# Kernel optimization log

Hardware: AMD Instinct MI355X
Metric: run time of the kernel (lower is better)

Reference implementation:

```python
import jax, jax.numpy as jnp
import numpy as np


def setup_inputs() -> dict:
    key = jax.random.key(0)
    k1, k2 = jax.random.split(key)
    B, S, H = 8, 2048, 1024
    lstm_output = jax.random.normal(k1, (B, S, H), dtype=jnp.float32)
    # xavier-uniform-like init for the bilinear weight
    limit = float(np.sqrt(6.0 / (H + H)))
    attention_weights = jax.random.uniform(k2, (H, H), dtype=jnp.float32, minval=-limit, maxval=limit)
    return {"lstm_output": lstm_output, "attention_weights": attention_weights}


def reference(lstm_output, attention_weights):
    # scores[b,i,j] = (x[b,i] @ W) . x[b,j]
    xw = jnp.einsum('bsh,hk->bsk', lstm_output, attention_weights)      # [B,S,H]
    scores = jnp.einsum('bsk,btk->bst', xw, lstm_output)                # [B,S,S]
    attn = jax.nn.softmax(scores, axis=-1)                              # [B,S,S]
    context = jnp.einsum('bst,bth->bsh', attn, lstm_output)             # [B,S,H]
    return (context, attn)
```

## Files before the change

kernel.cpp:

```cpp
#include <hip/hip_runtime.h>
#include <hip/hip_bf16.h>


#define BB 8
#define SS 2048
#define HH 1024

typedef __attribute__((ext_vector_type(8))) short bf16x8;
typedef __attribute__((ext_vector_type(4))) float f32x4;

__device__ __forceinline__ void async_load16(const void* gsrc, void* ldst) {
    typedef const unsigned int __attribute__((address_space(1)))* gp_t;
    typedef unsigned int __attribute__((address_space(3)))* lp_t;
    __builtin_amdgcn_global_load_lds((gp_t)gsrc, (lp_t)ldst, 16, 0, 0);
}

__device__ __forceinline__ unsigned short f2b(float f) {
    __hip_bfloat16 h = __float2bfloat16(f);
    return *(unsigned short*)&h;
}
__device__ __forceinline__ float b2f(unsigned short u) {
    __hip_bfloat16 h = *(__hip_bfloat16*)&u;
    return __bfloat162float(h);
}

__global__ __launch_bounds__(256) void split_x(const float* __restrict__ X,
                                               unsigned short* __restrict__ Xh,
                                               unsigned short* __restrict__ Xl) {
    const size_t i = ((size_t)blockIdx.x * 256 + threadIdx.x) * 8;
    float4 a = *(const float4*)(X + i);
    float4 b = *(const float4*)(X + i + 4);
    ushort4 h0, h1, l0, l1;
    float v, hf;
    v = a.x; h0.x = f2b(v); hf = b2f(h0.x); l0.x = f2b(v - hf);
    v = a.y; h0.y = f2b(v); hf = b2f(h0.y); l0.y = f2b(v - hf);
    v = a.z; h0.z = f2b(v); hf = b2f(h0.z); l0.z = f2b(v - hf);
    v = a.w; h0.w = f2b(v); hf = b2f(h0.w); l0.w = f2b(v - hf);
    v = b.x; h1.x = f2b(v); hf = b2f(h1.x); l1.x = f2b(v - hf);
    v = b.y; h1.y = f2b(v); hf = b2f(h1.y); l1.y = f2b(v - hf);
    v = b.z; h1.z = f2b(v); hf = b2f(h1.z); l1.z = f2b(v - hf);
    v = b.w; h1.w = f2b(v); hf = b2f(h1.w); l1.w = f2b(v - hf);
    *(ushort4*)(Xh + i) = h0; *(ushort4*)(Xh + i + 4) = h1;
    *(ushort4*)(Xl + i) = l0; *(ushort4*)(Xl + i + 4) = l1;
}

__global__ __launch_bounds__(256) void split_wT(const float* __restrict__ W,
                                                unsigned short* __restrict__ Th,
                                                unsigned short* __restrict__ Tl) {
    const int k0 = blockIdx.y * 64, n0 = blockIdx.x * 64;
    __shared__ float tile[64][65];
#pragma unroll
    for (int q = 0; q < 16; q++) {
        int idx = q * 256 + threadIdx.x;
        int r = idx >> 6, c = idx & 63;
        tile[r][c] = W[(size_t)(k0 + r) * HH + n0 + c];
    }
    __syncthreads();
#pragma unroll
    for (int q = 0; q < 16; q++) {
        int idx = q * 256 + threadIdx.x;
        int r = idx >> 6, c = idx & 63;
        float v = tile[c][r];
        unsigned short h = f2b(v);
        Th[(size_t)(n0 + r) * HH + k0 + c] = h;
        Tl[(size_t)(n0 + r) * HH + k0 + c] = f2b(v - b2f(h));
    }
}

__global__ __launch_bounds__(256) void gemm_xw3(const unsigned short* __restrict__ Ah,
                                                const unsigned short* __restrict__ Al,
                                                const unsigned short* __restrict__ Bh,
                                                const unsigned short* __restrict__ Bl,
                                                unsigned short* __restrict__ Ch,
                                                unsigned short* __restrict__ Cl) {
    const int b = blockIdx.z;
    const int i0 = blockIdx.y * 128, n0 = blockIdx.x * 128;
    const unsigned short* A_h = Ah + (size_t)b * SS * HH;
    const unsigned short* A_l = Al + (size_t)b * SS * HH;

    __shared__ __align__(16) unsigned short AsH[128 * 32];
    __shared__ __align__(16) unsigned short AsL[128 * 32];
    __shared__ __align__(16) unsigned short BsH[128 * 32];
    __shared__ __align__(16) unsigned short BsL[128 * 32];

    const int tid = threadIdx.x;
    const int wave = tid >> 6, lane = tid & 63;
    const int m16 = lane & 15, quad = lane >> 4;
    const int wy = wave >> 1, wx = wave & 1;
    const int rowA = tid >> 2;
    const int kq = (tid & 3) ^ ((rowA >> 1) & 3);

    f32x4 acc[4][4] = {};

    for (int k0 = 0; k0 < HH; k0 += 32) {
        const size_t ga0 = (size_t)(i0 + rowA) * HH + k0 + kq * 8;
        const size_t ga1 = (size_t)(i0 + 64 + rowA) * HH + k0 + kq * 8;
        const size_t gb0 = (size_t)(n0 + rowA) * HH + k0 + kq * 8;
        const size_t gb1 = (size_t)(n0 + 64 + rowA) * HH + k0 + kq * 8;
        async_load16(A_h + ga0, (char*)AsH + wave * 1024);
        async_load16(A_h + ga1, (char*)AsH + 4096 + wave * 1024);
        async_load16(A_l + ga0, (char*)AsL + wave * 1024);
        async_load16(A_l + ga1, (char*)AsL + 4096 + wave * 1024);
        async_load16(Bh + gb0, (char*)BsH + wave * 1024);
        async_load16(Bh + gb1, (char*)BsH + 4096 + wave * 1024);
        async_load16(Bl + gb0, (char*)BsL + wave * 1024);
        async_load16(Bl + gb1, (char*)BsL + 4096 + wave * 1024);
        __syncthreads();

        const int cs = quad ^ ((m16 >> 1) & 3);
        const int offA = (wy * 64 + m16) * 32 + cs * 8;
        const int offB = (wx * 64 + m16) * 32 + cs * 8;
        bf16x8 ah[4], al[4], bh[4], bl[4];
#pragma unroll
        for (int r = 0; r < 4; r++) {
            ah[r] = *(const bf16x8*)(AsH + offA + r * 16 * 32);
            al[r] = *(const bf16x8*)(AsL + offA + r * 16 * 32);
        }
#pragma unroll
        for (int c = 0; c < 4; c++) {
            bh[c] = *(const bf16x8*)(BsH + offB + c * 16 * 32);
            bl[c] = *(const bf16x8*)(BsL + offB + c * 16 * 32);
        }
#pragma unroll
        for (int r = 0; r < 4; r++)
#pragma unroll
            for (int c = 0; c < 4; c++) {
                acc[r][c] = __builtin_amdgcn_mfma_f32_16x16x32_bf16(ah[r], bh[c], acc[r][c], 0, 0, 0);
                acc[r][c] = __builtin_amdgcn_mfma_f32_16x16x32_bf16(ah[r], bl[c], acc[r][c], 0, 0, 0);
                acc[r][c] = __builtin_amdgcn_mfma_f32_16x16x32_bf16(al[r], bh[c], acc[r][c], 0, 0, 0);
            }
        __syncthreads();
    }

    unsigned short* ChB = Ch + (size_t)b * SS * HH;
    unsigned short* ClB = Cl + (size_t)b * SS * HH;
#pragma unroll
    for (int r = 0; r < 4; r++) {
        const int row = i0 + wy * 64 + r * 16 + quad * 4;
#pragma unroll
        for (int c = 0; c < 4; c++) {
            const int col = n0 + wx * 64 + c * 16 + m16;
#pragma unroll
            for (int reg = 0; reg < 4; reg++) {
                float v = acc[r][c][reg];
                unsigned short h = f2b(v);
                ChB[(size_t)(row + reg) * HH + col] = h;
                ClB[(size_t)(row + reg) * HH + col] = f2b(v - b2f(h));
            }
        }
    }
}

__global__ __launch_bounds__(512, 2) void gemm_sc3_8p(const unsigned short* __restrict__ Ah,
                                                      const unsigned short* __restrict__ Al,
                                                      const unsigned short* __restrict__ Bh,
                                                      const unsigned short* __restrict__ Bl,
                                                      float* __restrict__ SC) {
    const int b = blockIdx.z;
    const int i0 = blockIdx.y * 256, j0 = blockIdx.x * 256;
    const unsigned short* A_h = Ah + (size_t)b * SS * HH;
    const unsigned short* A_l = Al + (size_t)b * SS * HH;
    const unsigned short* B_h = Bh + (size_t)b * SS * HH;
    const unsigned short* B_l = Bl + (size_t)b * SS * HH;

    __shared__ __align__(16) unsigned short lds[65536];

    const int tid = threadIdx.x;
    const int wave = tid >> 6, lane = tid & 63;
    const int m16 = lane & 15, quad = lane >> 4;
    const int wy = wave >> 2, wx = wave & 3;
    const int rP = tid >> 2;
    const int kq = (tid & 3) ^ ((rP >> 1) & 3);
    const int cs = quad ^ ((m16 >> 1) & 3);
    const int wt16 = wave * 1024;
    const int rowA_off = (rP & 63) + ((rP >> 6) << 7);
    const int rowB_off = ((rP >> 5) << 6) + (rP & 31);

    const size_t aOff = (size_t)(i0 + rowA_off) * HH + kq * 8;
    const size_t bOff = (size_t)(j0 + rowB_off) * HH + kq * 8;

    f32x4 acc[2][4][2][2] = {};
    bf16x8 a_h[4], a_l[4], b_h[2][2], b_l[2][2];

#define STG_A(mh, kt, buf) do { \
        const size_t o_ = aOff + (size_t)(mh) * 64 * HH + (size_t)(kt) * 32; \
        async_load16(A_h + o_, (char*)lds + ((buf) * 32768 + (mh) * 4096) * 2 + wt16); \
        async_load16(A_l + o_, (char*)lds + ((buf) * 32768 + 8192 + (mh) * 4096) * 2 + wt16); \
    } while (0)
#define STG_B(nh, kt, buf) do { \
        const size_t o_ = bOff + (size_t)(nh) * 32 * HH + (size_t)(kt) * 32; \
        async_load16(B_h + o_, (char*)lds + ((buf) * 32768 + 16384 + (nh) * 4096) * 2 + wt16); \
        async_load16(B_l + o_, (char*)lds + ((buf) * 32768 + 24576 + (nh) * 4096) * 2 + wt16); \
    } while (0)
#define RD_A(mh, buf) do { \
        const int s0_ = (buf) * 32768 + ((mh) * 128 + wy * 64 + m16) * 32 + cs * 8; \
        _Pragma("unroll") for (int mi = 0; mi < 4; ++mi) { \
            a_h[mi] = *(const bf16x8*)&lds[s0_ + mi * 512]; \
            a_l[mi] = *(const bf16x8*)&lds[8192 + s0_ + mi * 512]; \
        } } while (0)
#define RD_B(nh, buf) do { \
        const int s0_ = (buf) * 32768 + ((nh) * 128 + wx * 32 + m16) * 32 + cs * 8; \
        _Pragma("unroll") for (int nj = 0; nj < 2; ++nj) { \
            b_h[nh][nj] = *(const bf16x8*)&lds[16384 + s0_ + nj * 512]; \
            b_l[nh][nj] = *(const bf16x8*)&lds[24576 + s0_ + nj * 512]; \
        } } while (0)
#define MFMA_PH(mh, nh) \
        __builtin_amdgcn_s_setprio(1); \
        _Pragma("unroll") for (int mi = 0; mi < 4; ++mi) \
        _Pragma("unroll") for (int nj = 0; nj < 2; ++nj) { \
            acc[mh][mi][nh][nj] = __builtin_amdgcn_mfma_f32_16x16x32_bf16(a_h[mi], b_h[nh][nj], acc[mh][mi][nh][nj], 0, 0, 0); \
            acc[mh][mi][nh][nj] = __builtin_amdgcn_mfma_f32_16x16x32_bf16(a_h[mi], b_l[nh][nj], acc[mh][mi][nh][nj], 0, 0, 0); \
            acc[mh][mi][nh][nj] = __builtin_amdgcn_mfma_f32_16x16x32_bf16(a_l[mi], b_h[nh][nj], acc[mh][mi][nh][nj], 0, 0, 0); \
        } \
        __builtin_amdgcn_s_setprio(0);

    STG_A(0, 0, 0); STG_A(1, 0, 0);
    STG_B(0, 0, 0); STG_B(1, 0, 0);
    STG_B(0, 1, 1); STG_B(1, 1, 1);
    asm volatile("s_waitcnt vmcnt(4)" ::: "memory");
    __builtin_amdgcn_s_barrier();
    RD_B(0, 0); RD_B(1, 0);

    for (int kt = 0; kt < 32; ++kt) {
        const int bufc = kt & 1, bufn = bufc ^ 1;
        const int ktA = kt < 31 ? kt + 1 : 31;
        const int ktB = kt < 30 ? kt + 2 : 31;
        RD_A(0, bufc);
        STG_A(0, ktA, bufn);
        __builtin_amdgcn_s_barrier();
        __builtin_amdgcn_sched_barrier(0);
        MFMA_PH(0, 0)
        __builtin_amdgcn_sched_barrier(0);
        __builtin_amdgcn_s_barrier();
        asm volatile("s_waitcnt vmcnt(6)" ::: "memory");
        STG_A(1, ktA, bufn);
        __builtin_amdgcn_s_barrier();
        __builtin_amdgcn_sched_barrier(0);
        MFMA_PH(0, 1)
        __builtin_amdgcn_sched_barrier(0);
        __builtin_amdgcn_s_barrier();
        asm volatile("s_waitcnt vmcnt(6)" ::: "memory");
        RD_A(1, bufc);
        STG_B(0, ktB, bufc);
        __builtin_amdgcn_s_barrier();
        __builtin_amdgcn_sched_barrier(0);
        MFMA_PH(1, 0)
        __builtin_amdgcn_sched_barrier(0);
        RD_B(0, bufn);
        __builtin_amdgcn_s_barrier();
        asm volatile("s_waitcnt vmcnt(4)" ::: "memory");
        STG_B(1, ktB, bufc);
        __builtin_amdgcn_s_barrier();
        __builtin_amdgcn_sched_barrier(0);
        MFMA_PH(1, 1)
        __builtin_amdgcn_sched_barrier(0);
        RD_B(1, bufn);
        __builtin_amdgcn_s_barrier();
    }

    float* Cb = SC + (size_t)b * SS * SS;
#pragma unroll
    for (int mh = 0; mh < 2; ++mh)
#pragma unroll
        for (int mi = 0; mi < 4; ++mi)
#pragma unroll
            for (int nh = 0; nh < 2; ++nh)
#pragma unroll
                for (int nj = 0; nj < 2; ++nj) {
                    const int row = i0 + wy * 128 + mh * 64 + mi * 16 + quad * 4;
                    const int col = j0 + wx * 64 + nh * 32 + nj * 16 + m16;
#pragma unroll
                    for (int reg = 0; reg < 4; ++reg)
                        Cb[(size_t)(row + reg) * SS + col] = acc[mh][mi][nh][nj][reg];
                }
#undef STG_A
#undef STG_B
#undef RD_A
#undef RD_B
#undef MFMA_PH
}

__global__ __launch_bounds__(256) void softmax_rows(float* __restrict__ P,
                                                    unsigned short* __restrict__ Pb) {
    const size_t row = blockIdx.x;
    float4* p4 = (float4*)(P + row * SS);
    const int tid = threadIdx.x;
    float4 v0 = p4[tid], v1 = p4[tid + 256];
    float m = fmaxf(fmaxf(fmaxf(v0.x, v0.y), fmaxf(v0.z, v0.w)),
                    fmaxf(fmaxf(v1.x, v1.y), fmaxf(v1.z, v1.w)));
#pragma unroll
    for (int off = 32; off; off >>= 1) m = fmaxf(m, __shfl_xor(m, off));
    __shared__ float red[4];
    const int wid = tid >> 6, lane = tid & 63;
    if (lane == 0) red[wid] = m;
    __syncthreads();
    m = fmaxf(fmaxf(red[0], red[1]), fmaxf(red[2], red[3]));
    v0.x = __expf(v0.x - m); v0.y = __expf(v0.y - m);
    v0.z = __expf(v0.z - m); v0.w = __expf(v0.w - m);
    v1.x = __expf(v1.x - m); v1.y = __expf(v1.y - m);
    v1.z = __expf(v1.z - m); v1.w = __expf(v1.w - m);
    float s = v0.x + v0.y + v0.z + v0.w + v1.x + v1.y + v1.z + v1.w;
#pragma unroll
    for (int off = 32; off; off >>= 1) s += __shfl_xor(s, off);
    __syncthreads();
    if (lane == 0) red[wid] = s;
    __syncthreads();
    s = red[0] + red[1] + red[2] + red[3];
    const float inv = 1.0f / s;
    v0.x *= inv; v0.y *= inv; v0.z *= inv; v0.w *= inv;
    v1.x *= inv; v1.y *= inv; v1.z *= inv; v1.w *= inv;
    p4[tid] = v0;
    p4[tid + 256] = v1;
    ushort4* b4 = (ushort4*)(Pb + row * SS);
    ushort4 u0 = { f2b(v0.x), f2b(v0.y), f2b(v0.z), f2b(v0.w) };
    ushort4 u1 = { f2b(v1.x), f2b(v1.y), f2b(v1.z), f2b(v1.w) };
    b4[tid] = u0;
    b4[tid + 256] = u1;
}

__global__ __launch_bounds__(256) void transpose_cvt(const float* __restrict__ X,
                                                     unsigned short* __restrict__ XT) {
    const int b = blockIdx.z;
    const int t0 = blockIdx.y * 64;
    const int h0 = blockIdx.x * 64;
    __shared__ float tile[64][65];
    const float* Xb = X + (size_t)b * SS * HH;
    unsigned short* Tb = XT + (size_t)b * HH * SS;
#pragma unroll
    for (int q = 0; q < 16; q++) {
        int idx = q * 256 + threadIdx.x;
        int r = idx >> 6, c = idx & 63;
        tile[r][c] = Xb[(size_t)(t0 + r) * HH + h0 + c];
    }
    __syncthreads();
#pragma unroll
    for (int q = 0; q < 16; q++) {
        int idx = q * 256 + threadIdx.x;
        int r = idx >> 6, c = idx & 63;
        Tb[(size_t)(h0 + r) * SS + t0 + c] = f2b(tile[c][r]);
    }
}

__global__ __launch_bounds__(256) void gemm_ctx_mfma(const unsigned short* __restrict__ Ab,
                                                     const unsigned short* __restrict__ Bt,
                                                     float* __restrict__ C) {
    const int b = blockIdx.z;
    const int i0 = blockIdx.y * 128;
    const int n0 = blockIdx.x * 128;
    const unsigned short* A = Ab + (size_t)b * SS * SS;
    const unsigned short* B = Bt + (size_t)b * HH * SS;

    __shared__ __align__(16) unsigned short As[128 * 32];
    __shared__ __align__(16) unsigned short Bs[128 * 32];

    const int tid = threadIdx.x;
    const int wave = tid >> 6, lane = tid & 63;
    const int m16 = lane & 15, quad = lane >> 4;
    const int wy = wave >> 1, wx = wave & 1;
    const int rowA = tid >> 2;
    const int kq = (tid & 3) ^ ((rowA >> 1) & 3);

    f32x4 acc[4][4] = {};

    for (int k0 = 0; k0 < SS; k0 += 32) {
        async_load16(A + (size_t)(i0 + rowA) * SS + k0 + kq * 8, (char*)As + wave * 1024);
        async_load16(A + (size_t)(i0 + 64 + rowA) * SS + k0 + kq * 8, (char*)As + 4096 + wave * 1024);
        async_load16(B + (size_t)(n0 + rowA) * SS + k0 + kq * 8, (char*)Bs + wave * 1024);
        async_load16(B + (size_t)(n0 + 64 + rowA) * SS + k0 + kq * 8, (char*)Bs + 4096 + wave * 1024);
        __syncthreads();

        const int cs = quad ^ ((m16 >> 1) & 3);
        const unsigned short* pA = As + (wy * 64 + m16) * 32 + cs * 8;
        const unsigned short* pB = Bs + (wx * 64 + m16) * 32 + cs * 8;
        bf16x8 af[4], bfr[4];
#pragma unroll
        for (int r = 0; r < 4; r++) af[r] = *(const bf16x8*)(pA + r * 16 * 32);
#pragma unroll
        for (int c = 0; c < 4; c++) bfr[c] = *(const bf16x8*)(pB + c * 16 * 32);
#pragma unroll
        for (int r = 0; r < 4; r++)
#pragma unroll
            for (int c = 0; c < 4; c++)
                acc[r][c] = __builtin_amdgcn_mfma_f32_16x16x32_bf16(af[r], bfr[c], acc[r][c], 0, 0, 0);
        __syncthreads();
    }

    float* Cb = C + (size_t)b * SS * HH;
#pragma unroll
    for (int r = 0; r < 4; r++) {
        const int row = i0 + wy * 64 + r * 16 + quad * 4;
#pragma unroll
        for (int c = 0; c < 4; c++) {
            const int col = n0 + wx * 64 + c * 16 + m16;
#pragma unroll
            for (int reg = 0; reg < 4; reg++)
                Cb[(size_t)(row + reg) * HH + col] = acc[r][c][reg];
        }
    }
}

extern "C" void kernel_launch(void* const* d_in, const int* in_sizes, int n_in,
                              void* d_out, int out_size, void* d_ws, size_t ws_size,
                              hipStream_t stream) {
    const float* X = (const float*)d_in[0];
    const float* W = (const float*)d_in[1];
    float* ctx  = (float*)d_out;
    float* attn = ctx + (size_t)BB * SS * HH;

    char* ws = (char*)d_ws;
    unsigned short* x_hi  = (unsigned short*)ws;
    unsigned short* x_lo  = (unsigned short*)(ws + ((size_t)32 << 20));
    unsigned short* wt_hi = (unsigned short*)(ws + ((size_t)64 << 20));
    unsigned short* wt_lo = (unsigned short*)(ws + ((size_t)66 << 20));
    unsigned short* xT     = x_hi;
    unsigned short* attn_b = x_lo;

    unsigned short* xw_hi = (unsigned short*)d_out;
    unsigned short* xw_lo = xw_hi + (size_t)BB * SS * HH;

    dim3 blk(256);
    split_x <<<dim3(BB * SS * HH / (8 * 256)), blk, 0, stream>>>(X, x_hi, x_lo);
    split_wT<<<dim3(HH / 64, HH / 64), blk, 0, stream>>>(W, wt_hi, wt_lo);
    gemm_xw3<<<dim3(HH / 128, SS / 128, BB), blk, 0, stream>>>(x_hi, x_lo, wt_hi, wt_lo, xw_hi, xw_lo);
    gemm_sc3_8p<<<dim3(SS / 256, SS / 256, BB), dim3(512), 0, stream>>>(xw_hi, xw_lo, x_hi, x_lo, attn);
    transpose_cvt<<<dim3(HH / 64, SS / 64, BB), blk, 0, stream>>>(X, xT);
    softmax_rows <<<dim3(BB * SS), blk, 0, stream>>>(attn, attn_b);
    gemm_ctx_mfma<<<dim3(HH / 128, SS / 128, BB), blk, 0, stream>>>(attn_b, xT, ctx);
}
```

Measured before the change: 679.8 us.

## Port XW and context GEMMs to the 256x256 eight-wave pipelined MFMA kernel

The XW projection and the context GEMM move from simple 128x128 single-buffered kernels onto the same 256x256, 512-thread, double-buffered, phase-interleaved pipeline already used for the score GEMM. That pipeline issues async global-to-LDS loads ahead of use, uses s_setprio around MFMA bursts, and gives each thread a larger output tile. The goal is to hide load latency, remove the per-k-step full barriers of the old kernels and raise data reuse per LDS byte. In exchange the kernels need more registers and LDS, and the grids get smaller (e.g. 4x8x8 blocks), which may leave fewer waves to fill the device.

Result: faster. 608.8 us (-10.5%).

```diff
diff --git a/kernel.cpp b/kernel.cpp
--- a/kernel.cpp
+++ b/kernel.cpp
@@ -67,101 +67,18 @@
     }
 }
 
-__global__ __launch_bounds__(256) void gemm_xw3(const unsigned short* __restrict__ Ah,
-                                                const unsigned short* __restrict__ Al,
-                                                const unsigned short* __restrict__ Bh,
-                                                const unsigned short* __restrict__ Bl,
-                                                unsigned short* __restrict__ Ch,
-                                                unsigned short* __restrict__ Cl) {
-    const int b = blockIdx.z;
-    const int i0 = blockIdx.y * 128, n0 = blockIdx.x * 128;
-    const unsigned short* A_h = Ah + (size_t)b * SS * HH;
-    const unsigned short* A_l = Al + (size_t)b * SS * HH;
-
-    __shared__ __align__(16) unsigned short AsH[128 * 32];
-    __shared__ __align__(16) unsigned short AsL[128 * 32];
-    __shared__ __align__(16) unsigned short BsH[128 * 32];
-    __shared__ __align__(16) unsigned short BsL[128 * 32];
-
-    const int tid = threadIdx.x;
-    const int wave = tid >> 6, lane = tid & 63;
-    const int m16 = lane & 15, quad = lane >> 4;
-    const int wy = wave >> 1, wx = wave & 1;
-    const int rowA = tid >> 2;
-    const int kq = (tid & 3) ^ ((rowA >> 1) & 3);
-
-    f32x4 acc[4][4] = {};
-
-    for (int k0 = 0; k0 < HH; k0 += 32) {
-        const size_t ga0 = (size_t)(i0 + rowA) * HH + k0 + kq * 8;
-        const size_t ga1 = (size_t)(i0 + 64 + rowA) * HH + k0 + kq * 8;
-        const size_t gb0 = (size_t)(n0 + rowA) * HH + k0 + kq * 8;
-        const size_t gb1 = (size_t)(n0 + 64 + rowA) * HH + k0 + kq * 8;
-        async_load16(A_h + ga0, (char*)AsH + wave * 1024);
-        async_load16(A_h + ga1, (char*)AsH + 4096 + wave * 1024);
-        async_load16(A_l + ga0, (char*)AsL + wave * 1024);
-        async_load16(A_l + ga1, (char*)AsL + 4096 + wave * 1024);
-        async_load16(Bh + gb0, (char*)BsH + wave * 1024);
-        async_load16(Bh + gb1, (char*)BsH + 4096 + wave * 1024);
-        async_load16(Bl + gb0, (char*)BsL + wave * 1024);
-        async_load16(Bl + gb1, (char*)BsL + 4096 + wave * 1024);
-        __syncthreads();
-
-        const int cs = quad ^ ((m16 >> 1) & 3);
-        const int offA = (wy * 64 + m16) * 32 + cs * 8;
-        const int offB = (wx * 64 + m16) * 32 + cs * 8;
-        bf16x8 ah[4], al[4], bh[4], bl[4];
-#pragma unroll
-        for (int r = 0; r < 4; r++) {
-            ah[r] = *(const bf16x8*)(AsH + offA + r * 16 * 32);
-            al[r] = *(const bf16x8*)(AsL + offA + r * 16 * 32);
-        }
-#pragma unroll
-        for (int c = 0; c < 4; c++) {
-            bh[c] = *(const bf16x8*)(BsH + offB + c * 16 * 32);
-            bl[c] = *(const bf16x8*)(BsL + offB + c * 16 * 32);
-        }
-#pragma unroll
-        for (int r = 0; r < 4; r++)
-#pragma unroll
-            for (int c = 0; c < 4; c++) {
-                acc[r][c] = __builtin_amdgcn_mfma_f32_16x16x32_bf16(ah[r], bh[c], acc[r][c], 0, 0, 0);
-                acc[r][c] = __builtin_amdgcn_mfma_f32_16x16x32_bf16(ah[r], bl[c], acc[r][c], 0, 0, 0);
-                acc[r][c] = __builtin_amdgcn_mfma_f32_16x16x32_bf16(al[r], bh[c], acc[r][c], 0, 0, 0);
-            }
-        __syncthreads();
-    }
-
-    unsigned short* ChB = Ch + (size_t)b * SS * HH;
-    unsigned short* ClB = Cl + (size_t)b * SS * HH;
-#pragma unroll
-    for (int r = 0; r < 4; r++) {
-        const int row = i0 + wy * 64 + r * 16 + quad * 4;
-#pragma unroll
-        for (int c = 0; c < 4; c++) {
-            const int col = n0 + wx * 64 + c * 16 + m16;
-#pragma unroll
-            for (int reg = 0; reg < 4; reg++) {
-                float v = acc[r][c][reg];
-                unsigned short h = f2b(v);
-                ChB[(size_t)(row + reg) * HH + col] = h;
-                ClB[(size_t)(row + reg) * HH + col] = f2b(v - b2f(h));
-            }
-        }
-    }
-}
-
-__global__ __launch_bounds__(512, 2) void gemm_sc3_8p(const unsigned short* __restrict__ Ah,
+__global__ __launch_bounds__(512, 2) void gemm_xw3_8p(const unsigned short* __restrict__ Ah,
                                                       const unsigned short* __restrict__ Al,
                                                       const unsigned short* __restrict__ Bh,
                                                       const unsigned short* __restrict__ Bl,
-                                                      float* __restrict__ SC) {
+                                                      unsigned short* __restrict__ Ch,
+                                                      unsigned short* __restrict__ Cl) {
     const int b = blockIdx.z;
     const int i0 = blockIdx.y * 256, j0 = blockIdx.x * 256;
     const unsigned short* A_h = Ah + (size_t)b * SS * HH;
     const unsigned short* A_l = Al + (size_t)b * SS * HH;
-    const unsigned short* B_h = Bh + (size_t)b * SS * HH;
-    const unsigned short* B_l = Bl + (size_t)b * SS * HH;
+    const unsigned short* B_h = Bh;
+    const unsigned short* B_l = Bl;
 
     __shared__ __align__(16) unsigned short lds[65536];
 
@@ -258,6 +175,140 @@
         __builtin_amdgcn_s_barrier();
     }
 
+    unsigned short* ChB = Ch + (size_t)b * SS * HH;
+    unsigned short* ClB = Cl + (size_t)b * SS * HH;
+#pragma unroll
+    for (int mh = 0; mh < 2; ++mh)
+#pragma unroll
+        for (int mi = 0; mi < 4; ++mi)
+#pragma unroll
+            for (int nh = 0; nh < 2; ++nh)
+#pragma unroll
+                for (int nj = 0; nj < 2; ++nj) {
+                    const int row = i0 + wy * 128 + mh * 64 + mi * 16 + quad * 4;
+                    const int col = j0 + wx * 64 + nh * 32 + nj * 16 + m16;
+#pragma unroll
+                    for (int reg = 0; reg < 4; ++reg) {
+                        float v = acc[mh][mi][nh][nj][reg];
+                        unsigned short h = f2b(v);
+                        ChB[(size_t)(row + reg) * HH + col] = h;
+                        ClB[(size_t)(row + reg) * HH + col] = f2b(v - b2f(h));
+                    }
+                }
+#undef STG_A
+#undef STG_B
+#undef RD_A
+#undef RD_B
+#undef MFMA_PH
+}
+
+__global__ __launch_bounds__(512, 2) void gemm_sc3_8p(const unsigned short* __restrict__ Ah,
+                                                      const unsigned short* __restrict__ Al,
+                                                      const unsigned short* __restrict__ Bh,
+                                                      const unsigned short* __restrict__ Bl,
+                                                      float* __restrict__ SC) {
+    const int b = blockIdx.z;
+    const int i0 = blockIdx.y * 256, j0 = blockIdx.x * 256;
+    const unsigned short* A_h = Ah + (size_t)b * SS * HH;
+    const unsigned short* A_l = Al + (size_t)b * SS * HH;
+    const unsigned short* B_h = Bh + (size_t)b * SS * HH;
+    const unsigned short* B_l = Bl + (size_t)b * SS * HH;
+
+    __shared__ __align__(16) unsigned short lds[65536];
+
+    const int tid = threadIdx.x;
+    const int wave = tid >> 6, lane = tid & 63;
+    const int m16 = lane & 15, quad = lane >> 4;
+    const int wy = wave >> 2, wx = wave & 3;
+    const int rP = tid >> 2;
+    const int kq = (tid & 3) ^ ((rP >> 1) & 3);
+    const int cs = quad ^ ((m16 >> 1) & 3);
+    const int wt16 = wave * 1024;
+    const int rowA_off = (rP & 63) + ((rP >> 6) << 7);
+    const int rowB_off = ((rP >> 5) << 6) + (rP & 31);
+
+    const size_t aOff = (size_t)(i0 + rowA_off) * HH + kq * 8;
+    const size_t bOff = (size_t)(j0 + rowB_off) * HH + kq * 8;
+
+    f32x4 acc[2][4][2][2] = {};
+    bf16x8 a_h[4], a_l[4], b_h[2][2], b_l[2][2];
+
+#define STG_A(mh, kt, buf) do { \
+        const size_t o_ = aOff + (size_t)(mh) * 64 * HH + (size_t)(kt) * 32; \
+        async_load16(A_h + o_, (char*)lds + ((buf) * 32768 + (mh) * 4096) * 2 + wt16); \
+        async_load16(A_l + o_, (char*)lds + ((buf) * 32768 + 8192 + (mh) * 4096) * 2 + wt16); \
+    } while (0)
+#define STG_B(nh, kt, buf) do { \
+        const size_t o_ = bOff + (size_t)(nh) * 32 * HH + (size_t)(kt) * 32; \
+        async_load16(B_h + o_, (char*)lds + ((buf) * 32768 + 16384 + (nh) * 4096) * 2 + wt16); \
+        async_load16(B_l + o_, (char*)lds + ((buf) * 32768 + 24576 + (nh) * 4096) * 2 + wt16); \
+    } while (0)
+#define RD_A(mh, buf) do { \
+        const int s0_ = (buf) * 32768 + ((mh) * 128 + wy * 64 + m16) * 32 + cs * 8; \
+        _Pragma("unroll") for (int mi = 0; mi < 4; ++mi) { \
+            a_h[mi] = *(const bf16x8*)&lds[s0_ + mi * 512]; \
+            a_l[mi] = *(const bf16x8*)&lds[8192 + s0_ + mi * 512]; \
+        } } while (0)
+#define RD_B(nh, buf) do { \
+        const int s0_ = (buf) * 32768 + ((nh) * 128 + wx * 32 + m16) * 32 + cs * 8; \
+        _Pragma("unroll") for (int nj = 0; nj < 2; ++nj) { \
+            b_h[nh][nj] = *(const bf16x8*)&lds[16384 + s0_ + nj * 512]; \
+            b_l[nh][nj] = *(const bf16x8*)&lds[24576 + s0_ + nj * 512]; \
+        } } while (0)
+#define MFMA_PH(mh, nh) \
+        __builtin_amdgcn_s_setprio(1); \
+        _Pragma("unroll") for (int mi = 0; mi < 4; ++mi) \
+        _Pragma("unroll") for (int nj = 0; nj < 2; ++nj) { \
+            acc[mh][mi][nh][nj] = __builtin_amdgcn_mfma_f32_16x16x32_bf16(a_h[mi], b_h[nh][nj], acc[mh][mi][nh][nj], 0, 0, 0); \
+            acc[mh][mi][nh][nj] = __builtin_amdgcn_mfma_f32_16x16x32_bf16(a_h[mi], b_l[nh][nj], acc[mh][mi][nh][nj], 0, 0, 0); \
+            acc[mh][mi][nh][nj] = __builtin_amdgcn_mfma_f32_16x16x32_bf16(a_l[mi], b_h[nh][nj], acc[mh][mi][nh][nj], 0, 0, 0); \
+        } \
+        __builtin_amdgcn_s_setprio(0);
+
+    STG_A(0, 0, 0); STG_A(1, 0, 0);
+    STG_B(0, 0, 0); STG_B(1, 0, 0);
+    STG_B(0, 1, 1); STG_B(1, 1, 1);
+    asm volatile("s_waitcnt vmcnt(4)" ::: "memory");
+    __builtin_amdgcn_s_barrier();
+    RD_B(0, 0); RD_B(1, 0);
+
+    for (int kt = 0; kt < 32; ++kt) {
+        const int bufc = kt & 1, bufn = bufc ^ 1;
+        const int ktA = kt < 31 ? kt + 1 : 31;
+        const int ktB = kt < 30 ? kt + 2 : 31;
+        RD_A(0, bufc);
+        STG_A(0, ktA, bufn);
+        __builtin_amdgcn_s_barrier();
+        __builtin_amdgcn_sched_barrier(0);
+        MFMA_PH(0, 0)
+        __builtin_amdgcn_sched_barrier(0);
+        __builtin_amdgcn_s_barrier();
+        asm volatile("s_waitcnt vmcnt(6)" ::: "memory");
+        STG_A(1, ktA, bufn);
+        __builtin_amdgcn_s_barrier();
+        __builtin_amdgcn_sched_barrier(0);
+        MFMA_PH(0, 1)
+        __builtin_amdgcn_sched_barrier(0);
+        __builtin_amdgcn_s_barrier();
+        asm volatile("s_waitcnt vmcnt(6)" ::: "memory");
+        RD_A(1, bufc);
+        STG_B(0, ktB, bufc);
+        __builtin_amdgcn_s_barrier();
+        __builtin_amdgcn_sched_barrier(0);
+        MFMA_PH(1, 0)
+        __builtin_amdgcn_sched_barrier(0);
+        RD_B(0, bufn);
+        __builtin_amdgcn_s_barrier();
+        asm volatile("s_waitcnt vmcnt(4)" ::: "memory");
+        STG_B(1, ktB, bufc);
+        __builtin_amdgcn_s_barrier();
+        __builtin_amdgcn_sched_barrier(0);
+        MFMA_PH(1, 1)
+        __builtin_amdgcn_sched_barrier(0);
+        RD_B(1, bufn);
+        __builtin_amdgcn_s_barrier();
+    }
+
     float* Cb = SC + (size_t)b * SS * SS;
 #pragma unroll
     for (int mh = 0; mh < 2; ++mh)
@@ -341,62 +392,127 @@
     }
 }
 
-__global__ __launch_bounds__(256) void gemm_ctx_mfma(const unsigned short* __restrict__ Ab,
-                                                     const unsigned short* __restrict__ Bt,
-                                                     float* __restrict__ C) {
+__global__ __launch_bounds__(512, 2) void gemm_ctx_8p(const unsigned short* __restrict__ Ab,
+                                                      const unsigned short* __restrict__ Bt,
+                                                      float* __restrict__ C) {
     const int b = blockIdx.z;
-    const int i0 = blockIdx.y * 128;
-    const int n0 = blockIdx.x * 128;
+    const int i0 = blockIdx.y * 256, n0 = blockIdx.x * 256;
     const unsigned short* A = Ab + (size_t)b * SS * SS;
     const unsigned short* B = Bt + (size_t)b * HH * SS;
 
-    __shared__ __align__(16) unsigned short As[128 * 32];
-    __shared__ __align__(16) unsigned short Bs[128 * 32];
+    __shared__ __align__(16) unsigned short lds[65536];
 
     const int tid = threadIdx.x;
     const int wave = tid >> 6, lane = tid & 63;
     const int m16 = lane & 15, quad = lane >> 4;
-    const int wy = wave >> 1, wx = wave & 1;
-    const int rowA = tid >> 2;
-    const int kq = (tid & 3) ^ ((rowA >> 1) & 3);
-
-    f32x4 acc[4][4] = {};
-
-    for (int k0 = 0; k0 < SS; k0 += 32) {
-        async_load16(A + (size_t)(i0 + rowA) * SS + k0 + kq * 8, (char*)As + wave * 1024);
-        async_load16(A + (size_t)(i0 + 64 + rowA) * SS + k0 + kq * 8, (char*)As + 4096 + wave * 1024);
-        async_load16(B + (size_t)(n0 + rowA) * SS + k0 + kq * 8, (char*)Bs + wave * 1024);
-        async_load16(B + (size_t)(n0 + 64 + rowA) * SS + k0 + kq * 8, (char*)Bs + 4096 + wave * 1024);
-        __syncthreads();
-
-        const int cs = quad ^ ((m16 >> 1) & 3);
-        const unsigned short* pA = As + (wy * 64 + m16) * 32 + cs * 8;
-        const unsigned short* pB = Bs + (wx * 64 + m16) * 32 + cs * 8;
-        bf16x8 af[4], bfr[4];
-#pragma unroll
-        for (int r = 0; r < 4; r++) af[r] = *(const bf16x8*)(pA + r * 16 * 32);
-#pragma unroll
-        for (int c = 0; c < 4; c++) bfr[c] = *(const bf16x8*)(pB + c * 16 * 32);
-#pragma unroll
-        for (int r = 0; r < 4; r++)
-#pragma unroll
-            for (int c = 0; c < 4; c++)
-                acc[r][c] = __builtin_amdgcn_mfma_f32_16x16x32_bf16(af[r], bfr[c], acc[r][c], 0, 0, 0);
-        __syncthreads();
+    const int m7 = m16 & 7;
+    const int wy = wave >> 2, wx = wave & 3;
+    const int rA8 = tid >> 3;
+    const int c8 = (tid & 7) ^ (rA8 & 7);
+    const int wt16 = wave * 1024;
+    const int sl0 = (quad ^ m7) * 8;
+    const int sl1 = ((quad + 4) ^ m7) * 8;
+
+    const size_t aSrc = (size_t)(i0 + rA8) * SS + c8 * 8;
+    const size_t bSrc = (size_t)(n0 + ((rA8 >> 5) << 6) + (rA8 & 31)) * SS + c8 * 8;
+
+    f32x4 acc[2][4][2][2] = {};
+    bf16x8 a[4][2], bb[2][2][2];
+
+#define CSTG_A(mh, h, kt, buf) \
+    async_load16(A + aSrc + (size_t)((mh) * 64 + (h) * 128) * SS + (size_t)(kt) * 64, \
+                 (char*)lds + (buf) * 65536 + (mh) * 16384 + (h) * 8192 + wt16)
+#define CSTG_B(nh, h, kt, buf) \
+    async_load16(B + bSrc + (size_t)((h) * 128 + (nh) * 32) * SS + (size_t)(kt) * 64, \
+                 (char*)lds + (buf) * 65536 + 32768 + (nh) * 16384 + (h) * 8192 + wt16)
+#define CRD_A(mh, buf) do { \
+        const int r0_ = (buf) * 32768 + ((mh) * 128 + wy * 64 + m16) * 64; \
+        _Pragma("unroll") for (int mi = 0; mi < 4; ++mi) { \
+            a[mi][0] = *(const bf16x8*)&lds[r0_ + mi * 1024 + sl0]; \
+            a[mi][1] = *(const bf16x8*)&lds[r0_ + mi * 1024 + sl1]; \
+        } } while (0)
+#define CRD_B(nh, buf) do { \
+        const int r0_ = (buf) * 32768 + 16384 + (nh) * 8192 + (wx * 32 + m16) * 64; \
+        _Pragma("unroll") for (int nj = 0; nj < 2; ++nj) { \
+            bb[nh][nj][0] = *(const bf16x8*)&lds[r0_ + nj * 1024 + sl0]; \
+            bb[nh][nj][1] = *(const bf16x8*)&lds[r0_ + nj * 1024 + sl1]; \
+        } } while (0)
+#define CMFMA(mh, nh) \
+        __builtin_amdgcn_s_setprio(1); \
+        _Pragma("unroll") for (int mi = 0; mi < 4; ++mi) \
+        _Pragma("unroll") for (int nj = 0; nj < 2; ++nj) { \
+            acc[mh][mi][nh][nj] = __builtin_amdgcn_mfma_f32_16x16x32_bf16(a[mi][0], bb[nh][nj][0], acc[mh][mi][nh][nj], 0, 0, 0); \
+            acc[mh][mi][nh][nj] = __builtin_amdgcn_mfma_f32_16x16x32_bf16(a[mi][1], bb[nh][nj][1], acc[mh][mi][nh][nj], 0, 0, 0); \
+        } \
+        __builtin_amdgcn_s_setprio(0);
+
+    CSTG_A(0, 0, 0, 0); CSTG_A(0, 1, 0, 0);
+    CSTG_A(1, 0, 0, 0); CSTG_A(1, 1, 0, 0);
+    CSTG_B(0, 0, 0, 0); CSTG_B(0, 1, 0, 0);
+    CSTG_B(1, 0, 0, 0); CSTG_B(1, 1, 0, 0);
+    CSTG_B(0, 0, 1, 1); CSTG_B(0, 1, 1, 1);
+    CSTG_B(1, 0, 1, 1); CSTG_B(1, 1, 1, 1);
+    asm volatile("s_waitcnt vmcnt(4)" ::: "memory");
+    __builtin_amdgcn_s_barrier();
+    CRD_B(0, 0); CRD_B(1, 0);
+
+    for (int kt = 0; kt < 32; ++kt) {
+        const int bufc = kt & 1, bufn = bufc ^ 1;
+        const int ktA = kt < 31 ? kt + 1 : 31;
+        const int ktB = kt < 30 ? kt + 2 : 31;
+        CRD_A(0, bufc);
+        CSTG_A(0, 0, ktA, bufn); CSTG_A(0, 1, ktA, bufn);
+        __builtin_amdgcn_s_barrier();
+        __builtin_amdgcn_sched_barrier(0);
+        CMFMA(0, 0)
+        __builtin_amdgcn_sched_barrier(0);
+        __builtin_amdgcn_s_barrier();
+        asm volatile("s_waitcnt vmcnt(6)" ::: "memory");
+        CSTG_A(1, 0, ktA, bufn); CSTG_A(1, 1, ktA, bufn);
+        __builtin_amdgcn_s_barrier();
+        __builtin_amdgcn_sched_barrier(0);
+        CMFMA(0, 1)
+        __builtin_amdgcn_sched_barrier(0);
+        __builtin_amdgcn_s_barrier();
+        asm volatile("s_waitcnt vmcnt(6)" ::: "memory");
+        CRD_A(1, bufc);
+        CSTG_B(0, 0, ktB, bufc); CSTG_B(0, 1, ktB, bufc);
+        __builtin_amdgcn_s_barrier();
+        __builtin_amdgcn_sched_barrier(0);
+        CMFMA(1, 0)
+        __builtin_amdgcn_sched_barrier(0);
+        CRD_B(0, bufn);
+        __builtin_amdgcn_s_barrier();
+        asm volatile("s_waitcnt vmcnt(4)" ::: "memory");
+        CSTG_B(1, 0, ktB, bufc); CSTG_B(1, 1, ktB, bufc);
+        __builtin_amdgcn_s_barrier();
+        __builtin_amdgcn_sched_barrier(0);
+        CMFMA(1, 1)
+        __builtin_amdgcn_sched_barrier(0);
+        CRD_B(1, bufn);
+        __builtin_amdgcn_s_barrier();
     }
 
     float* Cb = C + (size_t)b * SS * HH;
 #pragma unroll
-    for (int r = 0; r < 4; r++) {
-        const int row = i0 + wy * 64 + r * 16 + quad * 4;
-#pragma unroll
-        for (int c = 0; c < 4; c++) {
-            const int col = n0 + wx * 64 + c * 16 + m16;
-#pragma unroll
-            for (int reg = 0; reg < 4; reg++)
-                Cb[(size_t)(row + reg) * HH + col] = acc[r][c][reg];
-        }
-    }
+    for (int mh = 0; mh < 2; ++mh)
+#pragma unroll
+        for (int mi = 0; mi < 4; ++mi)
+#pragma unroll
+            for (int nh = 0; nh < 2; ++nh)
+#pragma unroll
+                for (int nj = 0; nj < 2; ++nj) {
+                    const int row = i0 + wy * 128 + mh * 64 + mi * 16 + quad * 4;
+                    const int col = n0 + wx * 64 + nh * 32 + nj * 16 + m16;
+#pragma unroll
+                    for (int reg = 0; reg < 4; ++reg)
+                        Cb[(size_t)(row + reg) * HH + col] = acc[mh][mi][nh][nj][reg];
+                }
+#undef CSTG_A
+#undef CSTG_B
+#undef CRD_A
+#undef CRD_B
+#undef CMFMA
 }
 
 extern "C" void kernel_launch(void* const* d_in, const int* in_sizes, int n_in,
@@ -421,9 +537,9 @@
     dim3 blk(256);
     split_x <<<dim3(BB * SS * HH / (8 * 256)), blk, 0, stream>>>(X, x_hi, x_lo);
     split_wT<<<dim3(HH / 64, HH / 64), blk, 0, stream>>>(W, wt_hi, wt_lo);
-    gemm_xw3<<<dim3(HH / 128, SS / 128, BB), blk, 0, stream>>>(x_hi, x_lo, wt_hi, wt_lo, xw_hi, xw_lo);
+    gemm_xw3_8p<<<dim3(HH / 256, SS / 256, BB), dim3(512), 0, stream>>>(x_hi, x_lo, wt_hi, wt_lo, xw_hi, xw_lo);
     gemm_sc3_8p<<<dim3(SS / 256, SS / 256, BB), dim3(512), 0, stream>>>(xw_hi, xw_lo, x_hi, x_lo, attn);
     transpose_cvt<<<dim3(HH / 64, SS / 64, BB), blk, 0, stream>>>(X, xT);
     softmax_rows <<<dim3(BB * SS), blk, 0, stream>>>(attn, attn_b);
-    gemm_ctx_mfma<<<dim3(HH / 128, SS / 128, BB), blk, 0, stream>>>(attn_b, xT, ctx);
-}
+    gemm_ctx_8p<<<dim3(HH / 256, SS / 256, BB), dim3(512), 0, stream>>>(attn_b, xT, ctx);
+}
```
